# Kernel tuning notes

Hardware: AMD Instinct MI355X
Metric: run time of the kernel (lower is better)

The kernel has to match this reference:

```python
import jax, jax.numpy as jnp
import numpy as np

NUM_EXPERTS = 64
TOPK = 8
EPS = 1.1920929e-07  # torch.finfo(float32).eps


def setup_inputs() -> dict:
    key = jax.random.key(0)
    k1, k2 = jax.random.split(key)
    hidden_states = jax.random.normal(k1, (1, 4096, 4096), dtype=jnp.float32)
    wg_weight = jax.random.normal(k2, (NUM_EXPERTS, 4096), dtype=jnp.float32) * 0.02
    return {"hidden_states": hidden_states, "wg_weight": wg_weight}


def _routing(logits, capacity):
    # logits: [T, E]; capacity: static python int
    gates = jax.nn.softmax(logits, axis=1)                       # [T, E]
    _, idx = jax.lax.top_k(gates, TOPK)                          # [T, k]
    emask = jax.nn.one_hot(idx, NUM_EXPERTS, dtype=jnp.float32)  # [T, k, E]
    # sum of selected gate probs per token, clamped at fp32 eps
    gates_s = jnp.clip(jnp.einsum('tke,te->t', emask, gates), EPS)[:, None]
    router_probs = gates / gates_s                               # [T, E]
    # priority: cumulative position of each token within each expert,
    # scanned over (topk-major, token-minor) flattened order
    idx_flat = idx.T.reshape(-1)                                 # [k*T]
    mflat = jax.nn.one_hot(idx_flat, NUM_EXPERTS, dtype=jnp.int32)
    tp = jnp.cumsum(mflat, axis=0) * mflat - 1                   # [k*T, E]
    tp = tp.reshape(TOPK, -1, NUM_EXPERTS).transpose(1, 0, 2).max(axis=1)  # [T, E]
    valid = (tp >= 0) & (tp < capacity)                          # [T, E]
    tp = jnp.where(valid, tp, 0)
    dispatch_mask = jax.nn.one_hot(tp, capacity, dtype=jnp.bool_) & valid[:, :, None]  # [T, E, C]
    combine_weights = router_probs[:, :, None] * dispatch_mask   # [T, E, C]
    return combine_weights, dispatch_mask


def reference(hidden_states, wg_weight):
    b, s, h = hidden_states.shape
    x = hidden_states.reshape(-1, h).astype(jnp.float32)         # [T, H]
    logits = x @ wg_weight.T                                     # [T, E]
    # expert_capacity = max tokens assigned to any expert (data-dependent,
    # computed eagerly as in the torch .item() call)
    _, idx = jax.lax.top_k(jax.nn.softmax(logits, axis=1), TOPK)
    counts = jnp.bincount(idx.reshape(-1), length=NUM_EXPERTS)
    capacity = int(counts.max())
    return _routing(logits, capacity)
```

## Files before the change

kernel.cpp:

```cpp
#include <hip/hip_runtime.h>
#include <hip/hip_bf16.h>


#define TOK 4096
#define HID 4096
#define NE  64
#define NK  8

__global__ __launch_bounds__(256) void gemm_splitk(
    const float* __restrict__ x, const float* __restrict__ wg,
    double* __restrict__ partial, int kchunk, int* __restrict__ flag) {
  __shared__ float xs[16][68];
  __shared__ float wsh[64][68];
  const int tid = threadIdx.x;
  if (blockIdx.x == 0 && blockIdx.y == 0 && tid == 0) *flag = 0;
  const int t0  = blockIdx.x * 16;
  const int k0  = blockIdx.y * kchunk;
  const int tok = tid & 15;
  const int eg  = tid >> 4;
  const int lrow = tid >> 4;
  const int lq   = tid & 15;
  double acc[4] = {0.0, 0.0, 0.0, 0.0};

  for (int s = 0; s < kchunk; s += 64) {
    const int kk = k0 + s;
    {
      float4 v = *(const float4*)&x[(size_t)(t0 + lrow) * HID + kk + lq * 4];
      *(float4*)&xs[lrow][lq * 4] = v;
    }
#pragma unroll
    for (int it = 0; it < 4; ++it) {
      int r = it * 16 + lrow;
      float4 v = *(const float4*)&wg[(size_t)r * HID + kk + lq * 4];
      *(float4*)&wsh[r][lq * 4] = v;
    }
    __syncthreads();
#pragma unroll
    for (int kc = 0; kc < 64; kc += 4) {
      float4 xv = *(const float4*)&xs[tok][kc];
#pragma unroll
      for (int j = 0; j < 4; ++j) {
        float4 wv = *(const float4*)&wsh[eg * 4 + j][kc];
        acc[j] = fma((double)xv.x, (double)wv.x, acc[j]);
        acc[j] = fma((double)xv.y, (double)wv.y, acc[j]);
        acc[j] = fma((double)xv.z, (double)wv.z, acc[j]);
        acc[j] = fma((double)xv.w, (double)wv.w, acc[j]);
      }
    }
    __syncthreads();
  }
  double* base = partial + (size_t)blockIdx.y * TOK * NE;
#pragma unroll
  for (int j = 0; j < 4; ++j)
    base[(size_t)(t0 + tok) * NE + eg * 4 + j] = acc[j];
}

__global__ __launch_bounds__(256) void verify_kernel(
    const float* __restrict__ x, const float* __restrict__ wg,
    const double* __restrict__ partial, int nsplit, int* __restrict__ flag) {
  const int gid  = blockIdx.x * blockDim.x + threadIdx.x;
  const int wid  = gid >> 6;
  const int lane = gid & 63;
  const int t = (wid * 521) & (TOK - 1);
  const int e = wid & 63;
  double acc = 0.0;
  for (int k = lane; k < HID; k += 64)
    acc = fma((double)x[(size_t)t * HID + k], (double)wg[(size_t)e * HID + k], acc);
#pragma unroll
  for (int off = 32; off; off >>= 1) acc += __shfl_xor(acc, off);
  if (lane == 0) {
    double got = 0.0;
    for (int p = 0; p < nsplit; ++p)
      got += partial[(size_t)p * TOK * NE + (size_t)t * NE + e];
    if (!(fabs(got - acc) <= 1e-6)) atomicOr(flag, 1);
  }
}

__global__ __launch_bounds__(256) void repair_gemm(
    const float* __restrict__ x, const float* __restrict__ wg,
    double* __restrict__ partial, int nsplit, const int* __restrict__ flag) {
  if (*(volatile const int*)flag == 0) return;
  const int gid = blockIdx.x * 256 + threadIdx.x;
  const int t = gid >> 6;
  const int e = gid & 63;
  double a0 = 0, a1 = 0, a2 = 0, a3 = 0, a4 = 0, a5 = 0, a6 = 0, a7 = 0;
  const float* xr = x  + (size_t)t * HID;
  const float* wr = wg + (size_t)e * HID;
  for (int k = 0; k < HID; k += 8) {
    float4 xv0 = *(const float4*)&xr[k];
    float4 xv1 = *(const float4*)&xr[k + 4];
    float4 wv0 = *(const float4*)&wr[k];
    float4 wv1 = *(const float4*)&wr[k + 4];
    a0 = fma((double)xv0.x, (double)wv0.x, a0);
    a1 = fma((double)xv0.y, (double)wv0.y, a1);
    a2 = fma((double)xv0.z, (double)wv0.z, a2);
    a3 = fma((double)xv0.w, (double)wv0.w, a3);
    a4 = fma((double)xv1.x, (double)wv1.x, a4);
    a5 = fma((double)xv1.y, (double)wv1.y, a5);
    a6 = fma((double)xv1.z, (double)wv1.z, a6);
    a7 = fma((double)xv1.w, (double)wv1.w, a7);
  }
  partial[(size_t)t * NE + e] =
      ((((((a0 + a1) + a2) + a3) + a4) + a5) + a6) + a7;
  for (int p = 1; p < nsplit; ++p)
    partial[(size_t)p * TOK * NE + (size_t)t * NE + e] = 0.0;
}

__global__ __launch_bounds__(256) void topk_kernel(
    const double* __restrict__ partial, int nsplit,
    int* __restrict__ idx_kt, float* __restrict__ w_kt) {
  const int gid  = blockIdx.x * blockDim.x + threadIdx.x;
  const int t    = gid >> 6;
  const int lane = gid & 63;

  double v = 0.0;
  for (int p = 0; p < nsplit; ++p)
    v += partial[(size_t)p * TOK * NE + (size_t)t * NE + lane];

  double m = v;
#pragma unroll
  for (int off = 32; off; off >>= 1) {
    double o = __shfl_xor(m, off);
    m = o > m ? o : m;
  }
  double g = exp(v - m);
  double s = g;
#pragma unroll
  for (int off = 32; off; off >>= 1) s += __shfl_xor(s, off);
  double gate = g / s;

  float key = (float)gate;
  double ssel = 0.0;
  int my_k = -1;
#pragma unroll
  for (int k = 0; k < NK; ++k) {
    float bv = key;
    int   bi = lane;
#pragma unroll
    for (int off = 32; off; off >>= 1) {
      float ov = __shfl_xor(bv, off);
      int   oi = __shfl_xor(bi, off);
      if (ov > bv || (ov == bv && oi < bi)) { bv = ov; bi = oi; }
    }
    ssel += __shfl(gate, bi);
    if (lane == bi) { my_k = k; key = -1.0f; }
  }
  double gs = ssel;
  const double eps = (double)1.1920929e-07f;
  if (gs < eps) gs = eps;

  if (my_k >= 0) {
    idx_kt[my_k * TOK + t] = lane;
    w_kt [my_k * TOK + t] = (float)(gate / gs);
  }
}

__global__ __launch_bounds__(1024) void rank_scatter(
    const int* __restrict__ idx_kt, const float* __restrict__ w_kt,
    float* __restrict__ out, int C) {
  const int e    = blockIdx.x;
  const int tid  = threadIdx.x;
  const int lane = tid & 63;
  const int w    = tid >> 6;
  __shared__ int wt[16];
  int running = 0;
  const unsigned long long below = (1ull << lane) - 1ull;

  for (int i0 = 0; i0 < NK * TOK; i0 += 1024) {
    const int i = i0 + tid;
    const bool mhit = (idx_kt[i] == e);
    unsigned long long mask = __ballot(mhit);
    if (lane == 0) wt[w] = __popcll(mask);
    __syncthreads();
    int woff = 0, tot = 0;
#pragma unroll
    for (int j = 0; j < 16; ++j) {
      int c = wt[j];
      tot += c;
      if (j < w) woff += c;
    }
    if (mhit) {
      const int c = running + woff + __popcll(mask & below);
      if (c < C) {
        const int t = i & (TOK - 1);
        size_t off = ((size_t)t * NE + e) * (size_t)C + (size_t)c;
        out[off] = w_kt[i];
        out[(size_t)TOK * NE * C + off] = 1.0f;
      }
    }
    running += tot;
    __syncthreads();
  }
}

extern "C" void kernel_launch(void* const* d_in, const int* in_sizes, int n_in,
                              void* d_out, int out_size, void* d_ws, size_t ws_size,
                              hipStream_t stream) {
  const float* x  = (const float*)d_in[0];
  const float* wg = (const float*)d_in[1];
  float* out = (float*)d_out;

  const int C = out_size / (2 * TOK * NE);

  const size_t slab = (size_t)TOK * NE * sizeof(double);
  const size_t tail = 2 * (size_t)NK * TOK * sizeof(int);
  int nsplit = 8;
  while (nsplit > 1 && (size_t)nsplit * slab + tail + 64 > ws_size) nsplit >>= 1;
  const int kchunk = HID / nsplit;

  char* ws = (char*)d_ws;
  double* partial = (double*)ws;
  int*    idx_kt  = (int*)  (ws + (size_t)nsplit * slab);
  float*  w_kt    = (float*)(ws + (size_t)nsplit * slab + (size_t)NK * TOK * 4);
  int*    flag    = (int*)  (ws + (size_t)nsplit * slab + tail);

  hipMemsetAsync(d_out, 0, (size_t)out_size * sizeof(float), stream);

  dim3 ggrid(TOK / 16, nsplit);
  gemm_splitk <<<ggrid, 256, 0, stream>>>(x, wg, partial, kchunk, flag);
  verify_kernel<<<128, 256, 0, stream>>>(x, wg, partial, nsplit, flag);
  repair_gemm <<<TOK * NE / 256, 256, 0, stream>>>(x, wg, partial, nsplit, flag);
  topk_kernel <<<TOK * 64 / 256, 256, 0, stream>>>(partial, nsplit, idx_kt, w_kt);
  rank_scatter<<<NE, 1024, 0, stream>>>(idx_kt, w_kt, out, C);
}
```

Measured before the change: 1.296 ms.

## Replace FP64 split-K gating GEMM with bf16x3 MFMA emulation plus FP64 fallback

The FP64-FMA split-K gating GEMM is replaced by a kernel that splits each fp32 operand into three bf16 parts and accumulates six cross-term products with bf16 MFMA instructions into fp32. Each block now covers 64 tokens instead of 16. The sampled verification tolerance is loosened from 1e-6 to 1e-3, and the fallback now reruns the full FP64 split-K GEMM only when that check fails. This moves the main compute off the slow FP64 path, but top-k routing decisions may change on near-tie gate values because sums are now accumulated in fp32.

```diff
diff --git a/kernel.cpp b/kernel.cpp
--- a/kernel.cpp
+++ b/kernel.cpp
@@ -7,52 +7,93 @@
 #define NE  64
 #define NK  8
 
-__global__ __launch_bounds__(256) void gemm_splitk(
+typedef __attribute__((ext_vector_type(8))) short short8;
+typedef __attribute__((ext_vector_type(4))) float f32x4;
+
+__device__ __forceinline__ short f2bf(float f) {
+  __hip_bfloat16 h = __float2bfloat16(f);
+  return *reinterpret_cast<short*>(&h);
+}
+__device__ __forceinline__ float bf2f(short s) {
+  unsigned u = ((unsigned)(unsigned short)s) << 16;
+  return __uint_as_float(u);
+}
+__device__ __forceinline__ void cvt3(float f, short& s0, short& s1, short& s2) {
+  s0 = f2bf(f);
+  float r1 = f - bf2f(s0);
+  s1 = f2bf(r1);
+  float r2 = r1 - bf2f(s1);
+  s2 = f2bf(r2);
+}
+
+__global__ __launch_bounds__(256) void gemm_bf16x3(
     const float* __restrict__ x, const float* __restrict__ wg,
     double* __restrict__ partial, int kchunk, int* __restrict__ flag) {
-  __shared__ float xs[16][68];
-  __shared__ float wsh[64][68];
+  __shared__ __align__(16) short XA[3][64][72];
+  __shared__ __align__(16) short WB[3][64][72];
   const int tid = threadIdx.x;
   if (blockIdx.x == 0 && blockIdx.y == 0 && tid == 0) *flag = 0;
-  const int t0  = blockIdx.x * 16;
-  const int k0  = blockIdx.y * kchunk;
-  const int tok = tid & 15;
-  const int eg  = tid >> 4;
-  const int lrow = tid >> 4;
-  const int lq   = tid & 15;
-  double acc[4] = {0.0, 0.0, 0.0, 0.0};
+  const int t0   = blockIdx.x * 64;
+  const int k0   = blockIdx.y * kchunk;
+  const int lane = tid & 63;
+  const int w    = tid >> 6;
+  const int m    = lane & 15;
+  const int q    = lane >> 4;
+  const int lrow = tid >> 2;
+  const int lq   = tid & 3;
+
+  f32x4 acc[4];
+#pragma unroll
+  for (int nt = 0; nt < 4; ++nt) acc[nt] = (f32x4){0.f, 0.f, 0.f, 0.f};
 
   for (int s = 0; s < kchunk; s += 64) {
     const int kk = k0 + s;
-    {
-      float4 v = *(const float4*)&x[(size_t)(t0 + lrow) * HID + kk + lq * 4];
-      *(float4*)&xs[lrow][lq * 4] = v;
-    }
-#pragma unroll
-    for (int it = 0; it < 4; ++it) {
-      int r = it * 16 + lrow;
-      float4 v = *(const float4*)&wg[(size_t)r * HID + kk + lq * 4];
-      *(float4*)&wsh[r][lq * 4] = v;
-    }
-    __syncthreads();
-#pragma unroll
-    for (int kc = 0; kc < 64; kc += 4) {
-      float4 xv = *(const float4*)&xs[tok][kc];
-#pragma unroll
-      for (int j = 0; j < 4; ++j) {
-        float4 wv = *(const float4*)&wsh[eg * 4 + j][kc];
-        acc[j] = fma((double)xv.x, (double)wv.x, acc[j]);
-        acc[j] = fma((double)xv.y, (double)wv.y, acc[j]);
-        acc[j] = fma((double)xv.z, (double)wv.z, acc[j]);
-        acc[j] = fma((double)xv.w, (double)wv.w, acc[j]);
+#pragma unroll
+    for (int c = 0; c < 4; ++c) {
+      const int col = lq * 16 + c * 4;
+      float4 xv = *(const float4*)&x [(size_t)(t0 + lrow) * HID + kk + col];
+      float4 wv = *(const float4*)&wg[(size_t)lrow * HID + kk + col];
+      short4 p0, p1, p2;
+      cvt3(xv.x, p0.x, p1.x, p2.x);  cvt3(xv.y, p0.y, p1.y, p2.y);
+      cvt3(xv.z, p0.z, p1.z, p2.z);  cvt3(xv.w, p0.w, p1.w, p2.w);
+      *(short4*)&XA[0][lrow][col] = p0;
+      *(short4*)&XA[1][lrow][col] = p1;
+      *(short4*)&XA[2][lrow][col] = p2;
+      cvt3(wv.x, p0.x, p1.x, p2.x);  cvt3(wv.y, p0.y, p1.y, p2.y);
+      cvt3(wv.z, p0.z, p1.z, p2.z);  cvt3(wv.w, p0.w, p1.w, p2.w);
+      *(short4*)&WB[0][lrow][col] = p0;
+      *(short4*)&WB[1][lrow][col] = p1;
+      *(short4*)&WB[2][lrow][col] = p2;
+    }
+    __syncthreads();
+#pragma unroll
+    for (int kc = 0; kc < 64; kc += 32) {
+      short8 a0 = *(const short8*)&XA[0][w * 16 + m][kc + q * 8];
+      short8 a1 = *(const short8*)&XA[1][w * 16 + m][kc + q * 8];
+      short8 a2 = *(const short8*)&XA[2][w * 16 + m][kc + q * 8];
+#pragma unroll
+      for (int nt = 0; nt < 4; ++nt) {
+        short8 b0 = *(const short8*)&WB[0][nt * 16 + m][kc + q * 8];
+        short8 b1 = *(const short8*)&WB[1][nt * 16 + m][kc + q * 8];
+        short8 b2 = *(const short8*)&WB[2][nt * 16 + m][kc + q * 8];
+        acc[nt] = __builtin_amdgcn_mfma_f32_16x16x32_bf16(a0, b0, acc[nt], 0, 0, 0);
+        acc[nt] = __builtin_amdgcn_mfma_f32_16x16x32_bf16(a0, b1, acc[nt], 0, 0, 0);
+        acc[nt] = __builtin_amdgcn_mfma_f32_16x16x32_bf16(a1, b0, acc[nt], 0, 0, 0);
+        acc[nt] = __builtin_amdgcn_mfma_f32_16x16x32_bf16(a0, b2, acc[nt], 0, 0, 0);
+        acc[nt] = __builtin_amdgcn_mfma_f32_16x16x32_bf16(a1, b1, acc[nt], 0, 0, 0);
+        acc[nt] = __builtin_amdgcn_mfma_f32_16x16x32_bf16(a2, b0, acc[nt], 0, 0, 0);
       }
     }
     __syncthreads();
   }
+
   double* base = partial + (size_t)blockIdx.y * TOK * NE;
 #pragma unroll
-  for (int j = 0; j < 4; ++j)
-    base[(size_t)(t0 + tok) * NE + eg * 4 + j] = acc[j];
+  for (int nt = 0; nt < 4; ++nt)
+#pragma unroll
+    for (int v = 0; v < 4; ++v)
+      base[(size_t)(t0 + w * 16 + q * 4 + v) * NE + nt * 16 + m] =
+          (double)acc[nt][v];
 }
 
 __global__ __launch_bounds__(256) void verify_kernel(
@@ -72,38 +113,56 @@
     double got = 0.0;
     for (int p = 0; p < nsplit; ++p)
       got += partial[(size_t)p * TOK * NE + (size_t)t * NE + e];
-    if (!(fabs(got - acc) <= 1e-6)) atomicOr(flag, 1);
-  }
-}
-
-__global__ __launch_bounds__(256) void repair_gemm(
+    if (!(fabs(got - acc) <= 1e-3)) atomicOr(flag, 1);
+  }
+}
+
+__global__ __launch_bounds__(256) void repair_splitk(
     const float* __restrict__ x, const float* __restrict__ wg,
-    double* __restrict__ partial, int nsplit, const int* __restrict__ flag) {
+    double* __restrict__ partial, int kchunk, const int* __restrict__ flag) {
   if (*(volatile const int*)flag == 0) return;
-  const int gid = blockIdx.x * 256 + threadIdx.x;
-  const int t = gid >> 6;
-  const int e = gid & 63;
-  double a0 = 0, a1 = 0, a2 = 0, a3 = 0, a4 = 0, a5 = 0, a6 = 0, a7 = 0;
-  const float* xr = x  + (size_t)t * HID;
-  const float* wr = wg + (size_t)e * HID;
-  for (int k = 0; k < HID; k += 8) {
-    float4 xv0 = *(const float4*)&xr[k];
-    float4 xv1 = *(const float4*)&xr[k + 4];
-    float4 wv0 = *(const float4*)&wr[k];
-    float4 wv1 = *(const float4*)&wr[k + 4];
-    a0 = fma((double)xv0.x, (double)wv0.x, a0);
-    a1 = fma((double)xv0.y, (double)wv0.y, a1);
-    a2 = fma((double)xv0.z, (double)wv0.z, a2);
-    a3 = fma((double)xv0.w, (double)wv0.w, a3);
-    a4 = fma((double)xv1.x, (double)wv1.x, a4);
-    a5 = fma((double)xv1.y, (double)wv1.y, a5);
-    a6 = fma((double)xv1.z, (double)wv1.z, a6);
-    a7 = fma((double)xv1.w, (double)wv1.w, a7);
-  }
-  partial[(size_t)t * NE + e] =
-      ((((((a0 + a1) + a2) + a3) + a4) + a5) + a6) + a7;
-  for (int p = 1; p < nsplit; ++p)
-    partial[(size_t)p * TOK * NE + (size_t)t * NE + e] = 0.0;
+  __shared__ float xs[16][68];
+  __shared__ float wsh[64][68];
+  const int tid = threadIdx.x;
+  const int t0  = blockIdx.x * 16;
+  const int k0  = blockIdx.y * kchunk;
+  const int tok = tid & 15;
+  const int eg  = tid >> 4;
+  const int lrow = tid >> 4;
+  const int lq   = tid & 15;
+  double acc[4] = {0.0, 0.0, 0.0, 0.0};
+
+  for (int s = 0; s < kchunk; s += 64) {
+    const int kk = k0 + s;
+    {
+      float4 v = *(const float4*)&x[(size_t)(t0 + lrow) * HID + kk + lq * 4];
+      *(float4*)&xs[lrow][lq * 4] = v;
+    }
+#pragma unroll
+    for (int it = 0; it < 4; ++it) {
+      int r = it * 16 + lrow;
+      float4 v = *(const float4*)&wg[(size_t)r * HID + kk + lq * 4];
+      *(float4*)&wsh[r][lq * 4] = v;
+    }
+    __syncthreads();
+#pragma unroll
+    for (int kc = 0; kc < 64; kc += 4) {
+      float4 xv = *(const float4*)&xs[tok][kc];
+#pragma unroll
+      for (int j = 0; j < 4; ++j) {
+        float4 wv = *(const float4*)&wsh[eg * 4 + j][kc];
+        acc[j] = fma((double)xv.x, (double)wv.x, acc[j]);
+        acc[j] = fma((double)xv.y, (double)wv.y, acc[j]);
+        acc[j] = fma((double)xv.z, (double)wv.z, acc[j]);
+        acc[j] = fma((double)xv.w, (double)wv.w, acc[j]);
+      }
+    }
+    __syncthreads();
+  }
+  double* base = partial + (size_t)blockIdx.y * TOK * NE;
+#pragma unroll
+  for (int j = 0; j < 4; ++j)
+    base[(size_t)(t0 + tok) * NE + eg * 4 + j] = acc[j];
 }
 
 __global__ __launch_bounds__(256) void topk_kernel(
@@ -216,10 +275,11 @@
 
   hipMemsetAsync(d_out, 0, (size_t)out_size * sizeof(float), stream);
 
-  dim3 ggrid(TOK / 16, nsplit);
-  gemm_splitk <<<ggrid, 256, 0, stream>>>(x, wg, partial, kchunk, flag);
+  dim3 bgrid(TOK / 64, nsplit);
+  dim3 rgrid(TOK / 16, nsplit);
+  gemm_bf16x3  <<<bgrid, 256, 0, stream>>>(x, wg, partial, kchunk, flag);
   verify_kernel<<<128, 256, 0, stream>>>(x, wg, partial, nsplit, flag);
-  repair_gemm <<<TOK * NE / 256, 256, 0, stream>>>(x, wg, partial, nsplit, flag);
-  topk_kernel <<<TOK * 64 / 256, 256, 0, stream>>>(partial, nsplit, idx_kt, w_kt);
-  rank_scatter<<<NE, 1024, 0, stream>>>(idx_kt, w_kt, out, C);
-}
+  repair_splitk<<<rgrid, 256, 0, stream>>>(x, wg, partial, kchunk, flag);
+  topk_kernel  <<<TOK * 64 / 256, 256, 0, stream>>>(partial, nsplit, idx_kt, w_kt);
+  rank_scatter <<<NE, 1024, 0, stream>>>(idx_kt, w_kt, out, C);
+}
```

Result: faster. 1.237 ms (-4.6%).
